# Performance work log

Measured on AMD Instinct MI355X. Metric: run time of the kernel, lower is better.

The kernel has to match this reference:

```python
import jax, jax.numpy as jnp
import numpy as np

IGNORE_IOU_THRESH = 0.7
EPS = 1e-12


def _batch_iou(bp, gt):
    """Pairwise IOU between bp [b,N,4] and gt [b,M,4], corner format -> [b,N,M]."""
    tl = jnp.maximum(bp[:, :, None, :2], gt[:, None, :, :2])  # [b,N,M,2]
    br = jnp.minimum(bp[:, :, None, 2:], gt[:, None, :, 2:])
    wh = jnp.clip(br - tl, 0.0)
    inter = wh[..., 0] * wh[..., 1]                           # [b,N,M]
    area_p = (bp[..., 2] - bp[..., 0]) * (bp[..., 3] - bp[..., 1])  # [b,N]
    area_g = (gt[..., 2] - gt[..., 0]) * (gt[..., 3] - gt[..., 1])  # [b,M]
    union = area_p[:, :, None] + area_g[:, None, :] - inter
    return inter / (union + EPS)


def setup_inputs() -> dict:
    key = jax.random.key(0)
    ks = jax.random.split(key, 7)
    b, N, M, C = 32, 22743, 50, 80
    return {
        "box_preds": jax.random.uniform(ks[0], (b, N, 4), dtype=jnp.float32),
        "gt_boxes": jax.random.uniform(ks[1], (b, M, 4), dtype=jnp.float32),
        "obj_t": jax.random.normal(ks[2], (b, N, 1), dtype=jnp.float32),
        "centers_t": jax.random.normal(ks[3], (b, N, 2), dtype=jnp.float32),
        "scales_t": jax.random.normal(ks[4], (b, N, 2), dtype=jnp.float32),
        "weights_t": jax.random.uniform(ks[5], (b, N, 2), dtype=jnp.float32),
        "clas_t": jax.random.uniform(ks[6], (b, N, C), dtype=jnp.float32),
    }


def reference(box_preds, gt_boxes, obj_t, centers_t, scales_t, weights_t, clas_t):
    b = box_preds.shape[0]
    bp = box_preds.reshape(b, -1, 4)
    # dynamic targets: objness = -(ious_max > thresh); centers/scales/weights = 0; class = -1
    ious = _batch_iou(bp, gt_boxes)                      # [b,N,M]
    ious_max = jnp.max(ious, axis=-1, keepdims=True)     # [b,N,1]
    dyn_obj = (ious_max > IGNORE_IOU_THRESH).astype(bp.dtype) * -1.0
    # masked merge of prefetched targets over dynamic targets
    mask = obj_t > 0                                     # [b,N,1], broadcasts
    objectness = jnp.where(mask, obj_t, dyn_obj)
    center_targets = jnp.where(mask, centers_t, 0.0)
    scale_targets = jnp.where(mask, scales_t, 0.0)
    weights = jnp.where(mask, weights_t, 0.0)
    class_targets = jnp.where(mask, clas_t, -1.0)
    class_mask = (mask & (class_targets >= 0)).astype(weights.dtype)
    return (objectness, center_targets, scale_targets, weights, class_targets, class_mask)
```

## Files before the change

kernel.cpp:

```cpp
#include <hip/hip_runtime.h>
#include <math.h>


__global__ __launch_bounds__(256) void rows_kernel(
    const float4* __restrict__ bp,
    const float4* __restrict__ gt,
    const float*  __restrict__ obj_t,
    const float2* __restrict__ cen,
    const float2* __restrict__ scl,
    const float2* __restrict__ wt,
    float*  __restrict__ out_obj,
    float2* __restrict__ out_cen,
    float2* __restrict__ out_scl,
    float2* __restrict__ out_wt,
    int N, int M)
{
    #pragma clang fp contract(off)
    __shared__ float4 sgt[64];
    const int b = blockIdx.y;
    if ((int)threadIdx.x < M) sgt[threadIdx.x] = gt[b * M + threadIdx.x];
    __syncthreads();

    const int n = blockIdx.x * blockDim.x + threadIdx.x;
    if (n >= N) return;
    const int idx = b * N + n;

    const float o    = obj_t[idx];
    const bool  mask = o > 0.0f;

    float objv = o;
    if (!mask) {
        const float4 p      = bp[idx];
        const float  area_p = (p.z - p.x) * (p.w - p.y);
        float m = -INFINITY;
        for (int j = 0; j < M; ++j) {
            const float4 g   = sgt[j];
            const float tlx  = fmaxf(p.x, g.x);
            const float tly  = fmaxf(p.y, g.y);
            const float brx  = fminf(p.z, g.z);
            const float bry  = fminf(p.w, g.w);
            const float w    = fmaxf(brx - tlx, 0.0f);
            const float h    = fmaxf(bry - tly, 0.0f);
            const float inter = w * h;
            const float area_g = (g.z - g.x) * (g.w - g.y);
            const float uni  = (area_p + area_g) - inter;
            const float iou  = inter / (uni + 1e-12f);
            m = fmaxf(m, iou);
        }
        objv = (m > 0.7f) ? -1.0f : 0.0f;
    }

    out_obj[idx] = objv;
    const float2 z2 = make_float2(0.0f, 0.0f);
    out_cen[idx] = mask ? cen[idx] : z2;
    out_scl[idx] = mask ? scl[idx] : z2;
    out_wt[idx]  = mask ? wt[idx]  : z2;
}

__global__ __launch_bounds__(256) void class_kernel(
    const float*  __restrict__ obj_t,
    const float4* __restrict__ clas,
    float4* __restrict__ out_ct,
    float4* __restrict__ out_cm,
    int total4)
{
    const int i = blockIdx.x * blockDim.x + threadIdx.x;
    if (i >= total4) return;
    const int row  = i / 20;
    const bool mask = obj_t[row] > 0.0f;

    float4 ct = make_float4(-1.0f, -1.0f, -1.0f, -1.0f);
    if (mask) ct = clas[i];

    float4 cm;
    cm.x = (mask && (ct.x >= 0.0f)) ? 1.0f : 0.0f;
    cm.y = (mask && (ct.y >= 0.0f)) ? 1.0f : 0.0f;
    cm.z = (mask && (ct.z >= 0.0f)) ? 1.0f : 0.0f;
    cm.w = (mask && (ct.w >= 0.0f)) ? 1.0f : 0.0f;

    out_ct[i] = ct;
    out_cm[i] = cm;
}

extern "C" void kernel_launch(void* const* d_in, const int* in_sizes, int n_in,
                              void* d_out, int out_size, void* d_ws, size_t ws_size,
                              hipStream_t stream) {
    const float* box_preds = (const float*)d_in[0];
    const float* gt_boxes  = (const float*)d_in[1];
    const float* obj_t     = (const float*)d_in[2];
    const float* centers_t = (const float*)d_in[3];
    const float* scales_t  = (const float*)d_in[4];
    const float* weights_t = (const float*)d_in[5];
    const float* clas_t    = (const float*)d_in[6];

    const int b  = 32;
    const int bN = in_sizes[2];
    const int N  = bN / b;
    const int M  = in_sizes[1] / (b * 4);

    float*  out     = (float*)d_out;
    float*  out_obj = out;
    float2* out_cen = (float2*)(out + (size_t)1  * bN);
    float2* out_scl = (float2*)(out + (size_t)3  * bN);
    float2* out_wt  = (float2*)(out + (size_t)5  * bN);
    float4* out_ct  = (float4*)(out + (size_t)7  * bN);
    float4* out_cm  = (float4*)(out + (size_t)87 * bN);

    dim3 grid1((N + 255) / 256, b);
    rows_kernel<<<grid1, 256, 0, stream>>>(
        (const float4*)box_preds, (const float4*)gt_boxes, obj_t,
        (const float2*)centers_t, (const float2*)scales_t,
        (const float2*)weights_t,
        out_obj, out_cen, out_scl, out_wt, N, M);

    const int total4 = bN * 20;
    class_kernel<<<(total4 + 255) / 256, 256, 0, stream>>>(
        obj_t, (const float4*)clas_t, out_ct, out_cm, total4);
}
```

Measured before the change: 649.3 us.

## Fuse row and class kernels into one with shared-memory mask

Merges the per-row IoU/target kernel and the class-target kernel into a single launch. Each block computes the mask for its 256 rows, shares it through LDS, then streams the matching 80-class slab with nontemporal loads and stores. This removes one launch and the re-read of obj_t. The cost is that the bandwidth-heavy class copy now shares blocks with the IoU compute, so each block does much more serial work and there are far fewer blocks in the grid.

```diff
diff --git a/kernel.cpp b/kernel.cpp
--- a/kernel.cpp
+++ b/kernel.cpp
@@ -2,84 +2,94 @@
 #include <math.h>
 
 
-__global__ __launch_bounds__(256) void rows_kernel(
+typedef float nfloat4 __attribute__((ext_vector_type(4)));
+
+__global__ __launch_bounds__(256) void yolo_fused_kernel(
     const float4* __restrict__ bp,
     const float4* __restrict__ gt,
     const float*  __restrict__ obj_t,
     const float2* __restrict__ cen,
     const float2* __restrict__ scl,
     const float2* __restrict__ wt,
+    const nfloat4* __restrict__ clas,
     float*  __restrict__ out_obj,
     float2* __restrict__ out_cen,
     float2* __restrict__ out_scl,
     float2* __restrict__ out_wt,
+    nfloat4* __restrict__ out_ct,
+    nfloat4* __restrict__ out_cm,
     int N, int M)
 {
     #pragma clang fp contract(off)
     __shared__ float4 sgt[64];
-    const int b = blockIdx.y;
-    if ((int)threadIdx.x < M) sgt[threadIdx.x] = gt[b * M + threadIdx.x];
+    __shared__ unsigned char smask[256];
+
+    const int bb = blockIdx.y;
+    if ((int)threadIdx.x < M) sgt[threadIdx.x] = gt[bb * M + threadIdx.x];
     __syncthreads();
 
-    const int n = blockIdx.x * blockDim.x + threadIdx.x;
-    if (n >= N) return;
-    const int idx = b * N + n;
+    const int n0 = blockIdx.x * 256;
+    const int n  = n0 + (int)threadIdx.x;
+    bool mask = false;
 
-    const float o    = obj_t[idx];
-    const bool  mask = o > 0.0f;
+    if (n < N) {
+        const int idx  = bb * N + n;
+        const float o  = obj_t[idx];
+        mask = o > 0.0f;
 
-    float objv = o;
-    if (!mask) {
-        const float4 p      = bp[idx];
-        const float  area_p = (p.z - p.x) * (p.w - p.y);
-        float m = -INFINITY;
-        for (int j = 0; j < M; ++j) {
-            const float4 g   = sgt[j];
-            const float tlx  = fmaxf(p.x, g.x);
-            const float tly  = fmaxf(p.y, g.y);
-            const float brx  = fminf(p.z, g.z);
-            const float bry  = fminf(p.w, g.w);
-            const float w    = fmaxf(brx - tlx, 0.0f);
-            const float h    = fmaxf(bry - tly, 0.0f);
-            const float inter = w * h;
-            const float area_g = (g.z - g.x) * (g.w - g.y);
-            const float uni  = (area_p + area_g) - inter;
-            const float iou  = inter / (uni + 1e-12f);
-            m = fmaxf(m, iou);
+        float objv = o;
+        if (!mask) {
+            const float4 p      = bp[idx];
+            const float  area_p = (p.z - p.x) * (p.w - p.y);
+            float m = -INFINITY;
+            for (int j = 0; j < M; ++j) {
+                const float4 g    = sgt[j];
+                const float tlx   = fmaxf(p.x, g.x);
+                const float tly   = fmaxf(p.y, g.y);
+                const float brx   = fminf(p.z, g.z);
+                const float bry   = fminf(p.w, g.w);
+                const float w     = fmaxf(brx - tlx, 0.0f);
+                const float h     = fmaxf(bry - tly, 0.0f);
+                const float inter = w * h;
+                const float area_g = (g.z - g.x) * (g.w - g.y);
+                const float uni   = (area_p + area_g) - inter;
+                const float iou   = inter / (uni + 1e-12f);
+                m = fmaxf(m, iou);
+            }
+            objv = (m > 0.7f) ? -1.0f : 0.0f;
         }
-        objv = (m > 0.7f) ? -1.0f : 0.0f;
+
+        out_obj[idx] = objv;
+        const float2 z2 = make_float2(0.0f, 0.0f);
+        out_cen[idx] = mask ? cen[idx] : z2;
+        out_scl[idx] = mask ? scl[idx] : z2;
+        out_wt[idx]  = mask ? wt[idx]  : z2;
     }
 
-    out_obj[idx] = objv;
-    const float2 z2 = make_float2(0.0f, 0.0f);
-    out_cen[idx] = mask ? cen[idx] : z2;
-    out_scl[idx] = mask ? scl[idx] : z2;
-    out_wt[idx]  = mask ? wt[idx]  : z2;
-}
+    smask[threadIdx.x] = mask ? 1 : 0;
+    __syncthreads();
 
-__global__ __launch_bounds__(256) void class_kernel(
-    const float*  __restrict__ obj_t,
-    const float4* __restrict__ clas,
-    float4* __restrict__ out_ct,
-    float4* __restrict__ out_cm,
-    int total4)
-{
-    const int i = blockIdx.x * blockDim.x + threadIdx.x;
-    if (i >= total4) return;
-    const int row  = i / 20;
-    const bool mask = obj_t[row] > 0.0f;
+    const int rows   = min(256, N - n0);
+    const int count4 = rows * 20;
+    const int base   = (bb * N + n0) * 20;
 
-    float4 ct = make_float4(-1.0f, -1.0f, -1.0f, -1.0f);
-    if (mask) ct = clas[i];
+    for (int k = (int)threadIdx.x; k < count4; k += 256) {
+        const int  lrow = k / 20;
+        const bool m2   = smask[lrow] != 0;
+        const int  gi   = base + k;
 
-    float4 cm;
-    cm.x = (mask && (ct.x >= 0.0f)) ? 1.0f : 0.0f;
-    cm.y = (mask && (ct.y >= 0.0f)) ? 1.0f : 0.0f;
-    cm.z = (mask && (ct.z >= 0.0f)) ? 1.0f : 0.0f;
-    cm.w = (mask && (ct.w >= 0.0f)) ? 1.0f : 0.0f;
+        nfloat4 ct = {-1.0f, -1.0f, -1.0f, -1.0f};
+        if (m2) ct = __builtin_nontemporal_load(&clas[gi]);
 
-    out_ct[i] = ct;
-    out_cm[i] = cm;
+        nfloat4 cm;
+        cm.x = (m2 && (ct.x >= 0.0f)) ? 1.0f : 0.0f;
+        cm.y = (m2 && (ct.y >= 0.0f)) ? 1.0f : 0.0f;
+        cm.z = (m2 && (ct.z >= 0.0f)) ? 1.0f : 0.0f;
+        cm.w = (m2 && (ct.w >= 0.0f)) ? 1.0f : 0.0f;
+
+        __builtin_nontemporal_store(ct, &out_ct[gi]);
+        __builtin_nontemporal_store(cm, &out_cm[gi]);
+    }
 }
 
 extern "C" void kernel_launch(void* const* d_in, const int* in_sizes, int n_in,
@@ -103,17 +113,13 @@
     float2* out_cen = (float2*)(out + (size_t)1  * bN);
     float2* out_scl = (float2*)(out + (size_t)3  * bN);
     float2* out_wt  = (float2*)(out + (size_t)5  * bN);
-    float4* out_ct  = (float4*)(out + (size_t)7  * bN);
-    float4* out_cm  = (float4*)(out + (size_t)87 * bN);
+    nfloat4* out_ct = (nfloat4*)(out + (size_t)7  * bN);
+    nfloat4* out_cm = (nfloat4*)(out + (size_t)87 * bN);
 
-    dim3 grid1((N + 255) / 256, b);
-    rows_kernel<<<grid1, 256, 0, stream>>>(
+    dim3 grid((N + 255) / 256, b);
+    yolo_fused_kernel<<<grid, 256, 0, stream>>>(
         (const float4*)box_preds, (const float4*)gt_boxes, obj_t,
         (const float2*)centers_t, (const float2*)scales_t,
-        (const float2*)weights_t,
-        out_obj, out_cen, out_scl, out_wt, N, M);
-
-    const int total4 = bN * 20;
-    class_kernel<<<(total4 + 255) / 256, 256, 0, stream>>>(
-        obj_t, (const float4*)clas_t, out_ct, out_cm, total4);
+        (const float2*)weights_t, (const nfloat4*)clas_t,
+        out_obj, out_cen, out_scl, out_wt, out_ct, out_cm, N, M);
 }
```

Result: no change. 651.6 us (+0.4%).
